# Kernel tuning notes

Measured on AMD Instinct MI355X. Metric: run time of the kernel, lower is better.

Reference implementation:

```python
import jax, jax.numpy as jnp
import numpy as np

TOKENS = 16384
INPUT_DIM = 2048
NUM_EXPERTS = 16
K = 2


def setup_inputs() -> dict:
    key = jax.random.key(0)
    kx, kn, kw, kb = jax.random.split(key, 4)
    x = jax.random.normal(kx, (TOKENS, INPUT_DIM), dtype=jnp.float32)
    noise = jax.random.normal(kn, (TOKENS, NUM_EXPERTS), dtype=jnp.float32)
    # nn.Linear params: weight [out, in], bias [out]; kaiming-uniform-ish init
    bound = 1.0 / np.sqrt(INPUT_DIM)
    W = jax.random.uniform(kw, (NUM_EXPERTS, INPUT_DIM), dtype=jnp.float32, minval=-bound, maxval=bound)
    b = jax.random.uniform(kb, (NUM_EXPERTS,), dtype=jnp.float32, minval=-bound, maxval=bound)
    return {"x": x, "noise": noise, "W": W, "b": b}


def reference(x, noise, W, b):
    # logits: [tokens, num_experts]
    logits = jnp.einsum("td,ed->te", x, W) + b
    noisy_logits = logits + noise * 0.1
    top_k_values, top_k_indices = jax.lax.top_k(noisy_logits, K)  # [tokens, K]
    weights = jax.nn.softmax(top_k_values, axis=-1)               # [tokens, K]
    # scatter weights back into dense [tokens, num_experts] (zeros elsewhere)
    one_hot = jax.nn.one_hot(top_k_indices, NUM_EXPERTS, dtype=logits.dtype)  # [tokens, K, E]
    sparse_weights = jnp.einsum("tke,tk->te", one_hot, weights)
    return sparse_weights
```

## Files before the change

kernel.cpp:

```cpp
#include <hip/hip_runtime.h>
#include <hip/hip_bf16.h>
#include <math.h>

#define TOKENS 16384
#define DIM    2048
#define NEXP   16

typedef float fvec4 __attribute__((ext_vector_type(4)));


__device__ __forceinline__ float fma4(fvec4 a, fvec4 w, float acc) {
    return fmaf(a.x, w.x, fmaf(a.y, w.y, fmaf(a.z, w.z, fmaf(a.w, w.w, acc))));
}

__global__ __launch_bounds__(256, 4) void gating_moe_kernel(
    const float* __restrict__ x,
    const float* __restrict__ noise,
    const float* __restrict__ W,
    const float* __restrict__ b,
    float* __restrict__ out)
{
    const int tid   = threadIdx.x;
    const int lane  = tid & 63;
    const int waveI = tid >> 6;
    const int sub   = lane & 31;
    const int tslot = lane >> 5;
    const int tokbase = blockIdx.x * 16 + waveI * 4;
    const int t0 = tokbase + tslot * 2;

    float acc0[NEXP], acc1[NEXP];
#pragma unroll
    for (int e = 0; e < NEXP; ++e) { acc0[e] = 0.0f; acc1[e] = 0.0f; }

    const fvec4* __restrict__ xr0 = (const fvec4*)(x + (size_t)t0 * DIM);
    const fvec4* __restrict__ xr1 = xr0 + (DIM / 4);
    const fvec4* __restrict__ Wv  = (const fvec4*)W;

#pragma unroll 2
    for (int j = 0; j < 16; ++j) {
        const int idx = j * 32 + sub;
        fvec4 xa = __builtin_nontemporal_load(&xr0[idx]);
        fvec4 xb = __builtin_nontemporal_load(&xr1[idx]);
        fvec4 wv[8];
#pragma unroll
        for (int e = 0; e < 8; ++e) wv[e] = Wv[e * (DIM / 4) + idx];
#pragma unroll
        for (int e = 0; e < 8; ++e) {
            acc0[e] = fma4(xa, wv[e], acc0[e]);
            acc1[e] = fma4(xb, wv[e], acc1[e]);
        }
#pragma unroll
        for (int e = 0; e < 8; ++e) wv[e] = Wv[(e + 8) * (DIM / 4) + idx];
#pragma unroll
        for (int e = 0; e < 8; ++e) {
            acc0[e + 8] = fma4(xa, wv[e], acc0[e + 8]);
            acc1[e + 8] = fma4(xb, wv[e], acc1[e + 8]);
        }
    }

#pragma unroll
    for (int e = 0; e < NEXP; ++e) {
        acc0[e] += __shfl_xor(acc0[e], 1);  acc1[e] += __shfl_xor(acc1[e], 1);
        acc0[e] += __shfl_xor(acc0[e], 2);  acc1[e] += __shfl_xor(acc1[e], 2);
        acc0[e] += __shfl_xor(acc0[e], 4);  acc1[e] += __shfl_xor(acc1[e], 4);
        acc0[e] += __shfl_xor(acc0[e], 8);  acc1[e] += __shfl_xor(acc1[e], 8);
    }
    const int r = (sub >> 4) & 1;
    float full[NEXP];
#pragma unroll
    for (int e = 0; e < NEXP; ++e) {
        float mine = r ? acc1[e] : acc0[e];
        float send = r ? acc0[e] : acc1[e];
        full[e] = mine + __shfl_xor(send, 16);
    }

    const int token = t0 + r;
    const fvec4* __restrict__ nz4 = (const fvec4*)(noise + (size_t)token * NEXP);
    float noisy[NEXP];
#pragma unroll
    for (int q = 0; q < 4; ++q) {
        fvec4 nv = __builtin_nontemporal_load(&nz4[q]);
        noisy[q * 4 + 0] = full[q * 4 + 0] + b[q * 4 + 0] + 0.1f * nv.x;
        noisy[q * 4 + 1] = full[q * 4 + 1] + b[q * 4 + 1] + 0.1f * nv.y;
        noisy[q * 4 + 2] = full[q * 4 + 2] + b[q * 4 + 2] + 0.1f * nv.z;
        noisy[q * 4 + 3] = full[q * 4 + 3] + b[q * 4 + 3] + 0.1f * nv.w;
    }

    float v1 = -INFINITY; int i1 = -1;
#pragma unroll
    for (int e = 0; e < NEXP; ++e) {
        bool g = noisy[e] > v1;
        v1 = g ? noisy[e] : v1;
        i1 = g ? e : i1;
    }
    float v2 = -INFINITY; int i2 = -1;
#pragma unroll
    for (int e = 0; e < NEXP; ++e) {
        bool g = (e != i1) && (noisy[e] > v2);
        v2 = g ? noisy[e] : v2;
        i2 = g ? e : i2;
    }

    float d  = __expf(v2 - v1);
    float w1 = 1.0f / (1.0f + d);
    float w2 = d * w1;

    const int e = sub & 15;
    float o = (e == i1) ? w1 : ((e == i2) ? w2 : 0.0f);
    out[(size_t)tokbase * NEXP + lane] = o;
}

extern "C" void kernel_launch(void* const* d_in, const int* in_sizes, int n_in,
                              void* d_out, int out_size, void* d_ws, size_t ws_size,
                              hipStream_t stream) {
    const float* x     = (const float*)d_in[0];
    const float* noise = (const float*)d_in[1];
    const float* W     = (const float*)d_in[2];
    const float* b     = (const float*)d_in[3];
    float* out = (float*)d_out;

    dim3 grid(TOKENS / 16);
    dim3 block(256);
    gating_moe_kernel<<<grid, block, 0, stream>>>(x, noise, W, b, out);
}
```

Measured before the change: 214.3 us.

## Process four tokens per half-wave to amortize W loads across more rows

Each 32-lane half-wave now computes four tokens instead of two, so every W vector it loads is reused across four x rows. The grid is halved and launch bounds drop to 2 blocks per SM so the larger 64-float accumulator set fits in registers. The reduction now uses a full 32-lane butterfly, and the output is written as float2 with 8 lanes per token. Non-temporal hints on the x and noise loads are dropped. Higher register use lowers occupancy, which may weaken latency hiding on this memory-bound streaming kernel.

```diff
diff --git a/kernel.cpp b/kernel.cpp
--- a/kernel.cpp
+++ b/kernel.cpp
@@ -13,7 +13,7 @@
     return fmaf(a.x, w.x, fmaf(a.y, w.y, fmaf(a.z, w.z, fmaf(a.w, w.w, acc))));
 }
 
-__global__ __launch_bounds__(256, 4) void gating_moe_kernel(
+__global__ __launch_bounds__(256, 2) void gating_moe_kernel(
     const float* __restrict__ x,
     const float* __restrict__ noise,
     const float* __restrict__ W,
@@ -24,62 +24,76 @@
     const int lane  = tid & 63;
     const int waveI = tid >> 6;
     const int sub   = lane & 31;
-    const int tslot = lane >> 5;
-    const int tokbase = blockIdx.x * 16 + waveI * 4;
-    const int t0 = tokbase + tslot * 2;
+    const int tgroup = lane >> 5;
+    const int wave_base = blockIdx.x * 32 + waveI * 8;
+    const int t0 = wave_base + tgroup * 4;
 
-    float acc0[NEXP], acc1[NEXP];
+    float acc[4][NEXP];
 #pragma unroll
-    for (int e = 0; e < NEXP; ++e) { acc0[e] = 0.0f; acc1[e] = 0.0f; }
+    for (int t = 0; t < 4; ++t)
+#pragma unroll
+        for (int e = 0; e < NEXP; ++e) acc[t][e] = 0.0f;
 
-    const fvec4* __restrict__ xr0 = (const fvec4*)(x + (size_t)t0 * DIM);
-    const fvec4* __restrict__ xr1 = xr0 + (DIM / 4);
-    const fvec4* __restrict__ Wv  = (const fvec4*)W;
+    const fvec4* __restrict__ xr = (const fvec4*)(x + (size_t)t0 * DIM);
+    const fvec4* __restrict__ Wv = (const fvec4*)W;
+    const int ROW = DIM / 4;
 
 #pragma unroll 2
     for (int j = 0; j < 16; ++j) {
         const int idx = j * 32 + sub;
-        fvec4 xa = __builtin_nontemporal_load(&xr0[idx]);
-        fvec4 xb = __builtin_nontemporal_load(&xr1[idx]);
+        fvec4 xv[4];
+#pragma unroll
+        for (int t = 0; t < 4; ++t) xv[t] = xr[t * ROW + idx];
+
         fvec4 wv[8];
 #pragma unroll
-        for (int e = 0; e < 8; ++e) wv[e] = Wv[e * (DIM / 4) + idx];
+        for (int e = 0; e < 8; ++e) wv[e] = Wv[e * ROW + idx];
 #pragma unroll
-        for (int e = 0; e < 8; ++e) {
-            acc0[e] = fma4(xa, wv[e], acc0[e]);
-            acc1[e] = fma4(xb, wv[e], acc1[e]);
-        }
+        for (int e = 0; e < 8; ++e)
 #pragma unroll
-        for (int e = 0; e < 8; ++e) wv[e] = Wv[(e + 8) * (DIM / 4) + idx];
+            for (int t = 0; t < 4; ++t)
+                acc[t][e] = fma4(xv[t], wv[e], acc[t][e]);
+
 #pragma unroll
-        for (int e = 0; e < 8; ++e) {
-            acc0[e + 8] = fma4(xa, wv[e], acc0[e + 8]);
-            acc1[e + 8] = fma4(xb, wv[e], acc1[e + 8]);
-        }
+        for (int e = 0; e < 8; ++e) wv[e] = Wv[(e + 8) * ROW + idx];
+#pragma unroll
+        for (int e = 0; e < 8; ++e)
+#pragma unroll
+            for (int t = 0; t < 4; ++t)
+                acc[t][e + 8] = fma4(xv[t], wv[e], acc[t][e + 8]);
     }
 
 #pragma unroll
-    for (int e = 0; e < NEXP; ++e) {
-        acc0[e] += __shfl_xor(acc0[e], 1);  acc1[e] += __shfl_xor(acc1[e], 1);
-        acc0[e] += __shfl_xor(acc0[e], 2);  acc1[e] += __shfl_xor(acc1[e], 2);
-        acc0[e] += __shfl_xor(acc0[e], 4);  acc1[e] += __shfl_xor(acc1[e], 4);
-        acc0[e] += __shfl_xor(acc0[e], 8);  acc1[e] += __shfl_xor(acc1[e], 8);
-    }
-    const int r = (sub >> 4) & 1;
+    for (int t = 0; t < 4; ++t)
+#pragma unroll
+        for (int e = 0; e < NEXP; ++e) {
+            float v = acc[t][e];
+            v += __shfl_xor(v, 1);
+            v += __shfl_xor(v, 2);
+            v += __shfl_xor(v, 4);
+            v += __shfl_xor(v, 8);
+            v += __shfl_xor(v, 16);
+            acc[t][e] = v;
+        }
+
+    const int tsel  = (lane >> 3) & 3;
+    const int token = wave_base + (lane >> 3);
+
     float full[NEXP];
 #pragma unroll
     for (int e = 0; e < NEXP; ++e) {
-        float mine = r ? acc1[e] : acc0[e];
-        float send = r ? acc0[e] : acc1[e];
-        full[e] = mine + __shfl_xor(send, 16);
+        float v = acc[0][e];
+        v = (tsel == 1) ? acc[1][e] : v;
+        v = (tsel == 2) ? acc[2][e] : v;
+        v = (tsel == 3) ? acc[3][e] : v;
+        full[e] = v;
     }
 
-    const int token = t0 + r;
     const fvec4* __restrict__ nz4 = (const fvec4*)(noise + (size_t)token * NEXP);
     float noisy[NEXP];
 #pragma unroll
     for (int q = 0; q < 4; ++q) {
-        fvec4 nv = __builtin_nontemporal_load(&nz4[q]);
+        fvec4 nv = nz4[q];
         noisy[q * 4 + 0] = full[q * 4 + 0] + b[q * 4 + 0] + 0.1f * nv.x;
         noisy[q * 4 + 1] = full[q * 4 + 1] + b[q * 4 + 1] + 0.1f * nv.y;
         noisy[q * 4 + 2] = full[q * 4 + 2] + b[q * 4 + 2] + 0.1f * nv.z;
@@ -105,9 +119,12 @@
     float w1 = 1.0f / (1.0f + d);
     float w2 = d * w1;
 
-    const int e = sub & 15;
-    float o = (e == i1) ? w1 : ((e == i2) ? w2 : 0.0f);
-    out[(size_t)tokbase * NEXP + lane] = o;
+    const int e0 = (lane & 7) * 2;
+    const int e1 = e0 + 1;
+    float o0 = (e0 == i1) ? w1 : ((e0 == i2) ? w2 : 0.0f);
+    float o1 = (e1 == i1) ? w1 : ((e1 == i2) ? w2 : 0.0f);
+    float2 o = make_float2(o0, o1);
+    ((float2*)(out + (size_t)token * NEXP))[lane & 7] = o;
 }
 
 extern "C" void kernel_launch(void* const* d_in, const int* in_sizes, int n_in,
@@ -119,7 +136,7 @@
     const float* b     = (const float*)d_in[3];
     float* out = (float*)d_out;
 
-    dim3 grid(TOKENS / 16);
+    dim3 grid(TOKENS / 32);
     dim3 block(256);
     gating_moe_kernel<<<grid, block, 0, stream>>>(x, noise, W, b, out);
 }
```

Result: no change. 211.3 us (-1.4%).
